# Performance work log

Measured on AMD Instinct MI355X. Metric: run time of the kernel, lower is better.

The kernel has to match this reference:

```python
import jax, jax.numpy as jnp
import numpy as np

N_Z = 128
N_COMP = 10
N_CLASSES = 10
BS = 8192


def setup_inputs() -> dict:
    key = jax.random.key(0)
    k_z, k_g, k_m = jax.random.split(key, 3)
    z = jax.random.normal(k_z, (BS, N_Z), dtype=jnp.float32)
    y = jax.random.randint(k_g, (BS,), 0, N_CLASSES, dtype=jnp.int64)
    # Gumbel noise replicating torch F.gumbel_softmax internal sampling
    gumbel = jax.random.gumbel(jax.random.fold_in(key, 1), (N_CLASSES, BS, N_COMP), dtype=jnp.float32)
    m = jax.random.normal(k_m, (N_CLASSES, N_COMP, N_Z), dtype=jnp.float32)
    # torch init: L = eye(n_z) per (class, component)
    L = jnp.broadcast_to(jnp.eye(N_Z, dtype=jnp.float32), (N_CLASSES, N_COMP, N_Z, N_Z))
    logits = jnp.zeros((N_CLASSES, N_COMP), dtype=jnp.float32)
    return {"z": z, "y": y, "gumbel": gumbel, "m": m, "L": L, "logits": logits}


def reference(z, y, gumbel, m, L, logits):
    C, K = logits.shape
    # hard gumbel-softmax (tau=1) per class, straight-through
    scores = logits[:, None, :] + gumbel                 # (C, bs, K)
    soft = jax.nn.softmax(scores, axis=-1)               # (C, bs, K)
    hard = jax.nn.one_hot(jnp.argmax(scores, axis=-1), K, dtype=soft.dtype)
    comp_mask = hard + soft - jax.lax.stop_gradient(soft)  # (C, bs, K)
    # every class/component affine: m + z @ L.T -> (C, K, bs, n_z)
    samps = jnp.einsum('bi,ckji->ckbj', z, L) + m[:, :, None, :]
    # select component per (class, sample)
    per_class = jnp.einsum('cbk,ckbj->cbj', comp_mask, samps)  # (C, bs, n_z)
    # select class per sample via one-hot(y)
    y1h = jax.nn.one_hot(y, C, dtype=per_class.dtype)          # (bs, C)
    x = jnp.einsum('bc,cbj->bj', y1h, per_class)               # (bs, n_z)
    return x
```

## Files before the change

### kernel.cpp

```cpp
#include <hip/hip_runtime.h>


#define N_Z 128
#define N_COMP 10
#define N_CLASSES 10
#define N_CK (N_CLASSES * N_COMP)
#define ZCAP 96
#define LIST_CAP 256

typedef __attribute__((ext_vector_type(4))) __bf16 bf16x4;
typedef __attribute__((ext_vector_type(8))) __bf16 bf16x8;
typedef __attribute__((ext_vector_type(4))) float f32x4;

__global__ __launch_bounds__(64) void k_select(
    const int* __restrict__ y, const float* __restrict__ gumbel,
    const float* __restrict__ logits, unsigned char* __restrict__ ck_arr, int bs)
{
    int b = blockIdx.x * 64 + threadIdx.x;
    if (b >= bs) return;
    int c = y[b];
    const float* g  = gumbel + ((size_t)c * bs + b) * N_COMP;
    const float* lg = logits + c * N_COMP;
    float best = g[0] + lg[0];
    int bi = 0;
    #pragma unroll
    for (int k = 1; k < N_COMP; ++k) {
        float s = g[k] + lg[k];
        if (s > best) { best = s; bi = k; }
    }
    ck_arr[b] = (unsigned char)(c * N_COMP + bi);
}

__global__ __launch_bounds__(256) void k_mfma(
    const float* __restrict__ z, const float* __restrict__ m,
    const float* __restrict__ L, const unsigned char* __restrict__ ck_arr,
    float* __restrict__ out, int bs)
{
    const int ck = blockIdx.x;
    const int jh = blockIdx.y;

    __shared__ __align__(16) __bf16 Lsb[64 * 128];
    __shared__ __align__(16) __bf16 zsb[ZCAP * 128];
    __shared__ int list[LIST_CAP];
    __shared__ int cnt;

    const int t = threadIdx.x;
    if (t == 0) cnt = 0;

    {
        const float4* Lg4 = (const float4*)(L + ((size_t)ck * N_Z + jh * 64) * N_Z);
        #pragma unroll
        for (int p = 0; p < 8; ++p) {
            int f = p * 256 + t;
            float4 v = Lg4[f];
            bf16x4 b4 = { (__bf16)v.x, (__bf16)v.y, (__bf16)v.z, (__bf16)v.w };
            *(bf16x4*)&Lsb[f * 4] = b4;
        }
    }
    __syncthreads();

    {
        const uint4* ck4 = (const uint4*)ck_arr;
        #pragma unroll
        for (int p = 0; p < 2; ++p) {
            int idx = p * 256 + t;
            uint4 v = ck4[idx];
            int b0 = idx * 16;
            unsigned w[4] = {v.x, v.y, v.z, v.w};
            #pragma unroll
            for (int q = 0; q < 4; ++q) {
                #pragma unroll
                for (int e = 0; e < 4; ++e) {
                    if (((w[q] >> (8 * e)) & 0xFFu) == (unsigned)ck) {
                        int p2 = atomicAdd(&cnt, 1);
                        if (p2 < LIST_CAP) list[p2] = b0 + q * 4 + e;
                    }
                }
            }
        }
    }
    __syncthreads();

    const int n = min(cnt, LIST_CAP);

    const int wv   = t >> 6;
    const int lane = t & 63;
    const int mn   = lane & 15;
    const int quad = lane >> 4;

    for (int s0 = 0; s0 < n; s0 += ZCAP) {
        const int ns = min(ZCAP, n - s0);

        #pragma unroll
        for (int p = 0; p < 12; ++p) {
            int f   = p * 256 + t;
            int row = f >> 5;
            if (row < ns) {
                int samp = list[s0 + row];
                float4 v = *(const float4*)(z + (size_t)samp * N_Z + (f & 31) * 4);
                bf16x4 b4 = { (__bf16)v.x, (__bf16)v.y, (__bf16)v.z, (__bf16)v.w };
                *(bf16x4*)&zsb[row * 128 + (f & 31) * 4] = b4;
            }
        }
        __syncthreads();

        const int ntiles = (ns + 15) >> 4;
        #pragma unroll
        for (int half = 0; half < 2; ++half) {
            int nt = wv + half * 4;
            if (nt >= ntiles) break;
            int nb = nt * 16;
            int srow = nb + mn;

            bf16x8 bf[4];
            #pragma unroll
            for (int ks = 0; ks < 4; ++ks)
                bf[ks] = *(const bf16x8*)&zsb[srow * 128 + ks * 32 + quad * 8];

            #pragma unroll
            for (int mt = 0; mt < 4; ++mt) {
                f32x4 acc = {0.f, 0.f, 0.f, 0.f};
                #pragma unroll
                for (int ks = 0; ks < 4; ++ks) {
                    bf16x8 af = *(const bf16x8*)&Lsb[(mt * 16 + mn) * 128 + ks * 32 + quad * 8];
                    acc = __builtin_amdgcn_mfma_f32_16x16x32_bf16(af, bf[ks], acc, 0, 0, 0);
                }
                int sidx = nb + mn;
                if (sidx < ns) {
                    int samp = list[s0 + sidx];
                    int j0 = jh * 64 + mt * 16 + quad * 4;
                    float4 mv = *(const float4*)(m + ck * N_Z + j0);
                    float4 o;
                    o.x = acc.x + mv.x;
                    o.y = acc.y + mv.y;
                    o.z = acc.z + mv.z;
                    o.w = acc.w + mv.w;
                    *(float4*)(out + (size_t)samp * N_Z + j0) = o;
                }
            }
        }
        __syncthreads();
    }
}

extern "C" void kernel_launch(void* const* d_in, const int* in_sizes, int n_in,
                              void* d_out, int out_size, void* d_ws, size_t ws_size,
                              hipStream_t stream)
{
    const float* z      = (const float*)d_in[0];
    const int*   y      = (const int*)d_in[1];
    const float* gumbel = (const float*)d_in[2];
    const float* m      = (const float*)d_in[3];
    const float* L      = (const float*)d_in[4];
    const float* logits = (const float*)d_in[5];
    float* out = (float*)d_out;

    const int bs = in_sizes[0] / N_Z;

    unsigned char* ck_arr = (unsigned char*)d_ws;

    k_select<<<(bs + 63) / 64, 64, 0, stream>>>(y, gumbel, logits, ck_arr, bs);
    k_mfma<<<dim3(N_CK, 2), 256, 0, stream>>>(z, m, L, ck_arr, out, bs);
}
```

Measured before the change: 84.83 us.

## Fuse select and MFMA kernels into one cooperative kernel with grid sync

Merges the component-selection kernel into the matmul kernel by launching a cooperative grid of 400 blocks, where the first blocks compute the per-sample class/component index, followed by a grid-wide barrier. The output-column split is also doubled from 2 to 4 quarters, so each block loads a 32-row slice of L and runs half as many MFMA tiles. The aim is to remove the second kernel launch and gap and to add parallelism. In exchange it adds a grid sync, and it repeats the per-block sample list scan and z gather across twice as many blocks.

Result: slower. 143.4 us (+69.1%).

```diff
diff --git a/kernel.cpp b/kernel.cpp
--- a/kernel.cpp
+++ b/kernel.cpp
@@ -1,4 +1,7 @@
 #include <hip/hip_runtime.h>
+#include <hip/hip_cooperative_groups.h>
+
+namespace cg = cooperative_groups;
 
 
 #define N_Z 128
@@ -12,52 +15,53 @@
 typedef __attribute__((ext_vector_type(8))) __bf16 bf16x8;
 typedef __attribute__((ext_vector_type(4))) float f32x4;
 
-__global__ __launch_bounds__(64) void k_select(
-    const int* __restrict__ y, const float* __restrict__ gumbel,
-    const float* __restrict__ logits, unsigned char* __restrict__ ck_arr, int bs)
+__global__ __launch_bounds__(256) void k_coop(
+    const float* __restrict__ z, const int* __restrict__ y,
+    const float* __restrict__ gumbel, const float* __restrict__ m,
+    const float* __restrict__ L, const float* __restrict__ logits,
+    float* __restrict__ out, unsigned char* __restrict__ ck_arr, int bs)
 {
-    int b = blockIdx.x * 64 + threadIdx.x;
-    if (b >= bs) return;
-    int c = y[b];
-    const float* g  = gumbel + ((size_t)c * bs + b) * N_COMP;
-    const float* lg = logits + c * N_COMP;
-    float best = g[0] + lg[0];
-    int bi = 0;
-    #pragma unroll
-    for (int k = 1; k < N_COMP; ++k) {
-        float s = g[k] + lg[k];
-        if (s > best) { best = s; bi = k; }
-    }
-    ck_arr[b] = (unsigned char)(c * N_COMP + bi);
-}
+    const int ck  = blockIdx.x;
+    const int jq  = blockIdx.y;
+    const int t   = threadIdx.x;
+    const int bid = blockIdx.y * gridDim.x + blockIdx.x;
 
-__global__ __launch_bounds__(256) void k_mfma(
-    const float* __restrict__ z, const float* __restrict__ m,
-    const float* __restrict__ L, const unsigned char* __restrict__ ck_arr,
-    float* __restrict__ out, int bs)
-{
-    const int ck = blockIdx.x;
-    const int jh = blockIdx.y;
-
-    __shared__ __align__(16) __bf16 Lsb[64 * 128];
+    __shared__ __align__(16) __bf16 Lsb[32 * 128];
     __shared__ __align__(16) __bf16 zsb[ZCAP * 128];
     __shared__ int list[LIST_CAP];
     __shared__ int cnt;
 
-    const int t = threadIdx.x;
     if (t == 0) cnt = 0;
 
     {
-        const float4* Lg4 = (const float4*)(L + ((size_t)ck * N_Z + jh * 64) * N_Z);
+        const float4* Lg4 = (const float4*)(L + ((size_t)ck * N_Z + jq * 32) * N_Z);
         #pragma unroll
-        for (int p = 0; p < 8; ++p) {
+        for (int p = 0; p < 4; ++p) {
             int f = p * 256 + t;
             float4 v = Lg4[f];
             bf16x4 b4 = { (__bf16)v.x, (__bf16)v.y, (__bf16)v.z, (__bf16)v.w };
             *(bf16x4*)&Lsb[f * 4] = b4;
         }
     }
-    __syncthreads();
+
+    const int nselblk = bs >> 8;
+    if (bid < nselblk) {
+        int b = bid * 256 + t;
+        int c = y[b];
+        const float* g  = gumbel + ((size_t)c * bs + b) * N_COMP;
+        const float* lg = logits + c * N_COMP;
+        float best = g[0] + lg[0];
+        int bi = 0;
+        #pragma unroll
+        for (int k = 1; k < N_COMP; ++k) {
+            float s = g[k] + lg[k];
+            if (s > best) { best = s; bi = k; }
+        }
+        ck_arr[b] = (unsigned char)(c * N_COMP + bi);
+        __threadfence();
+    }
+
+    cg::this_grid().sync();
 
     {
         const uint4* ck4 = (const uint4*)ck_arr;
@@ -118,7 +122,7 @@
                 bf[ks] = *(const bf16x8*)&zsb[srow * 128 + ks * 32 + quad * 8];
 
             #pragma unroll
-            for (int mt = 0; mt < 4; ++mt) {
+            for (int mt = 0; mt < 2; ++mt) {
                 f32x4 acc = {0.f, 0.f, 0.f, 0.f};
                 #pragma unroll
                 for (int ks = 0; ks < 4; ++ks) {
@@ -128,7 +132,7 @@
                 int sidx = nb + mn;
                 if (sidx < ns) {
                     int samp = list[s0 + sidx];
-                    int j0 = jh * 64 + mt * 16 + quad * 4;
+                    int j0 = jq * 32 + mt * 16 + quad * 4;
                     float4 mv = *(const float4*)(m + ck * N_Z + j0);
                     float4 o;
                     o.x = acc.x + mv.x;
@@ -155,10 +159,12 @@
     const float* logits = (const float*)d_in[5];
     float* out = (float*)d_out;
 
-    const int bs = in_sizes[0] / N_Z;
-
+    int bs = in_sizes[0] / N_Z;
     unsigned char* ck_arr = (unsigned char*)d_ws;
 
-    k_select<<<(bs + 63) / 64, 64, 0, stream>>>(y, gumbel, logits, ck_arr, bs);
-    k_mfma<<<dim3(N_CK, 2), 256, 0, stream>>>(z, m, L, ck_arr, out, bs);
+    void* args[] = { (void*)&z, (void*)&y, (void*)&gumbel, (void*)&m,
+                     (void*)&L, (void*)&logits, (void*)&out, (void*)&ck_arr,
+                     (void*)&bs };
+    hipLaunchCooperativeKernel((const void*)k_coop, dim3(N_CK, 4), dim3(256),
+                               args, 0, stream);
 }
```

## Load z rows directly into MFMA registers and overlap L loads with selection

Applied to the files above, without the earlier changes.

The MFMA kernel drops the shared-memory staging buffer for z. Each wave now gathers its 16 sample rows straight from global memory into bf16 fragments, which removes the chunk loop and its barriers. The loads of L and of the ck array are issued before the selection scan, so their latency overlaps it, and the L tile gets a padded pitch to avoid LDS bank conflicts. k_select now uses 256-thread blocks with float2 loads of the gumbel noise. The cost is uncoalesced per-lane z reads and higher register pressure from holding L in registers.

Measured after the change: 80.64 us. 1.05x faster.

```diff
diff --git a/kernel.cpp b/kernel.cpp
--- a/kernel.cpp
+++ b/kernel.cpp
@@ -5,29 +5,36 @@
 #define N_COMP 10
 #define N_CLASSES 10
 #define N_CK (N_CLASSES * N_COMP)
-#define ZCAP 96
+#define LPITCH 136
 #define LIST_CAP 256
 
 typedef __attribute__((ext_vector_type(4))) __bf16 bf16x4;
 typedef __attribute__((ext_vector_type(8))) __bf16 bf16x8;
 typedef __attribute__((ext_vector_type(4))) float f32x4;
 
-__global__ __launch_bounds__(64) void k_select(
+__global__ __launch_bounds__(256) void k_select(
     const int* __restrict__ y, const float* __restrict__ gumbel,
     const float* __restrict__ logits, unsigned char* __restrict__ ck_arr, int bs)
 {
-    int b = blockIdx.x * 64 + threadIdx.x;
+    int b = blockIdx.x * 256 + threadIdx.x;
     if (b >= bs) return;
     int c = y[b];
     const float* g  = gumbel + ((size_t)c * bs + b) * N_COMP;
     const float* lg = logits + c * N_COMP;
-    float best = g[0] + lg[0];
+    float2 g01 = *(const float2*)(g + 0);
+    float2 g23 = *(const float2*)(g + 2);
+    float2 g45 = *(const float2*)(g + 4);
+    float2 g67 = *(const float2*)(g + 6);
+    float2 g89 = *(const float2*)(g + 8);
+    float sc[N_COMP] = {
+        g01.x + lg[0], g01.y + lg[1], g23.x + lg[2], g23.y + lg[3],
+        g45.x + lg[4], g45.y + lg[5], g67.x + lg[6], g67.y + lg[7],
+        g89.x + lg[8], g89.y + lg[9] };
+    float best = sc[0];
     int bi = 0;
     #pragma unroll
-    for (int k = 1; k < N_COMP; ++k) {
-        float s = g[k] + lg[k];
-        if (s > best) { best = s; bi = k; }
-    }
+    for (int k = 1; k < N_COMP; ++k)
+        if (sc[k] > best) { best = sc[k]; bi = k; }
     ck_arr[b] = (unsigned char)(c * N_COMP + bi);
 }
 
@@ -39,107 +46,95 @@
     const int ck = blockIdx.x;
     const int jh = blockIdx.y;
 
-    __shared__ __align__(16) __bf16 Lsb[64 * 128];
-    __shared__ __align__(16) __bf16 zsb[ZCAP * 128];
+    __shared__ __align__(16) __bf16 Lsb[64 * LPITCH];
     __shared__ int list[LIST_CAP];
     __shared__ int cnt;
 
     const int t = threadIdx.x;
     if (t == 0) cnt = 0;
 
+    uint4 ckw[2];
+    {
+        const uint4* ck4 = (const uint4*)ck_arr;
+        ckw[0] = ck4[t];
+        ckw[1] = ck4[256 + t];
+    }
+    float4 lv[8];
     {
         const float4* Lg4 = (const float4*)(L + ((size_t)ck * N_Z + jh * 64) * N_Z);
         #pragma unroll
-        for (int p = 0; p < 8; ++p) {
-            int f = p * 256 + t;
-            float4 v = Lg4[f];
-            bf16x4 b4 = { (__bf16)v.x, (__bf16)v.y, (__bf16)v.z, (__bf16)v.w };
-            *(bf16x4*)&Lsb[f * 4] = b4;
-        }
+        for (int p = 0; p < 8; ++p) lv[p] = Lg4[p * 256 + t];
     }
     __syncthreads();
 
-    {
-        const uint4* ck4 = (const uint4*)ck_arr;
+    #pragma unroll
+    for (int h = 0; h < 2; ++h) {
+        int b0 = (h * 256 + t) * 16;
+        unsigned w[4] = {ckw[h].x, ckw[h].y, ckw[h].z, ckw[h].w};
         #pragma unroll
-        for (int p = 0; p < 2; ++p) {
-            int idx = p * 256 + t;
-            uint4 v = ck4[idx];
-            int b0 = idx * 16;
-            unsigned w[4] = {v.x, v.y, v.z, v.w};
+        for (int q = 0; q < 4; ++q) {
             #pragma unroll
-            for (int q = 0; q < 4; ++q) {
-                #pragma unroll
-                for (int e = 0; e < 4; ++e) {
-                    if (((w[q] >> (8 * e)) & 0xFFu) == (unsigned)ck) {
-                        int p2 = atomicAdd(&cnt, 1);
-                        if (p2 < LIST_CAP) list[p2] = b0 + q * 4 + e;
-                    }
+            for (int e = 0; e < 4; ++e) {
+                if (((w[q] >> (8 * e)) & 0xFFu) == (unsigned)ck) {
+                    int p2 = atomicAdd(&cnt, 1);
+                    if (p2 < LIST_CAP) list[p2] = b0 + q * 4 + e;
                 }
             }
         }
     }
+    #pragma unroll
+    for (int p = 0; p < 8; ++p) {
+        int f   = p * 256 + t;
+        int row = f >> 5;
+        int c4  = f & 31;
+        bf16x4 b4 = { (__bf16)lv[p].x, (__bf16)lv[p].y, (__bf16)lv[p].z, (__bf16)lv[p].w };
+        *(bf16x4*)&Lsb[row * LPITCH + c4 * 4] = b4;
+    }
     __syncthreads();
 
     const int n = min(cnt, LIST_CAP);
+    const int ntiles = (n + 15) >> 4;
 
     const int wv   = t >> 6;
     const int lane = t & 63;
     const int mn   = lane & 15;
     const int quad = lane >> 4;
 
-    for (int s0 = 0; s0 < n; s0 += ZCAP) {
-        const int ns = min(ZCAP, n - s0);
+    for (int nt = wv; nt < ntiles; nt += 4) {
+        const int nb = nt * 16;
+        const int sidx = nb + mn;
+        const int samp = list[sidx < n ? sidx : n - 1];
+        const float* zrow = z + (size_t)samp * N_Z;
+
+        bf16x8 bf[4];
+        #pragma unroll
+        for (int ks = 0; ks < 4; ++ks) {
+            float4 z0 = *(const float4*)(zrow + ks * 32 + quad * 8);
+            float4 z1 = *(const float4*)(zrow + ks * 32 + quad * 8 + 4);
+            bf16x8 b8 = { (__bf16)z0.x, (__bf16)z0.y, (__bf16)z0.z, (__bf16)z0.w,
+                          (__bf16)z1.x, (__bf16)z1.y, (__bf16)z1.z, (__bf16)z1.w };
+            bf[ks] = b8;
+        }
 
         #pragma unroll
-        for (int p = 0; p < 12; ++p) {
-            int f   = p * 256 + t;
-            int row = f >> 5;
-            if (row < ns) {
-                int samp = list[s0 + row];
-                float4 v = *(const float4*)(z + (size_t)samp * N_Z + (f & 31) * 4);
-                bf16x4 b4 = { (__bf16)v.x, (__bf16)v.y, (__bf16)v.z, (__bf16)v.w };
-                *(bf16x4*)&zsb[row * 128 + (f & 31) * 4] = b4;
+        for (int mt = 0; mt < 4; ++mt) {
+            f32x4 acc = {0.f, 0.f, 0.f, 0.f};
+            #pragma unroll
+            for (int ks = 0; ks < 4; ++ks) {
+                bf16x8 af = *(const bf16x8*)&Lsb[(mt * 16 + mn) * LPITCH + ks * 32 + quad * 8];
+                acc = __builtin_amdgcn_mfma_f32_16x16x32_bf16(af, bf[ks], acc, 0, 0, 0);
+            }
+            if (sidx < n) {
+                int j0 = jh * 64 + mt * 16 + quad * 4;
+                float4 mv = *(const float4*)(m + ck * N_Z + j0);
+                float4 o;
+                o.x = acc.x + mv.x;
+                o.y = acc.y + mv.y;
+                o.z = acc.z + mv.z;
+                o.w = acc.w + mv.w;
+                *(float4*)(out + (size_t)list[sidx] * N_Z + j0) = o;
             }
         }
-        __syncthreads();
-
-        const int ntiles = (ns + 15) >> 4;
-        #pragma unroll
-        for (int half = 0; half < 2; ++half) {
-            int nt = wv + half * 4;
-            if (nt >= ntiles) break;
-            int nb = nt * 16;
-            int srow = nb + mn;
-
-            bf16x8 bf[4];
-            #pragma unroll
-            for (int ks = 0; ks < 4; ++ks)
-                bf[ks] = *(const bf16x8*)&zsb[srow * 128 + ks * 32 + quad * 8];
-
-            #pragma unroll
-            for (int mt = 0; mt < 4; ++mt) {
-                f32x4 acc = {0.f, 0.f, 0.f, 0.f};
-                #pragma unroll
-                for (int ks = 0; ks < 4; ++ks) {
-                    bf16x8 af = *(const bf16x8*)&Lsb[(mt * 16 + mn) * 128 + ks * 32 + quad * 8];
-                    acc = __builtin_amdgcn_mfma_f32_16x16x32_bf16(af, bf[ks], acc, 0, 0, 0);
-                }
-                int sidx = nb + mn;
-                if (sidx < ns) {
-                    int samp = list[s0 + sidx];
-                    int j0 = jh * 64 + mt * 16 + quad * 4;
-                    float4 mv = *(const float4*)(m + ck * N_Z + j0);
-                    float4 o;
-                    o.x = acc.x + mv.x;
-                    o.y = acc.y + mv.y;
-                    o.z = acc.z + mv.z;
-                    o.w = acc.w + mv.w;
-                    *(float4*)(out + (size_t)samp * N_Z + j0) = o;
-                }
-            }
-        }
-        __syncthreads();
     }
 }
 
@@ -159,6 +154,6 @@
 
     unsigned char* ck_arr = (unsigned char*)d_ws;
 
-    k_select<<<(bs + 63) / 64, 64, 0, stream>>>(y, gumbel, logits, ck_arr, bs);
+    k_select<<<(bs + 255) / 256, 256, 0, stream>>>(y, gumbel, logits, ck_arr, bs);
     k_mfma<<<dim3(N_CK, 2), 256, 0, stream>>>(z, m, L, ck_arr, out, bs);
 }
```
